# Performance work log

Measured on AMD Instinct MI355X. Metric: run time of the kernel, lower is better.

The kernel has to match this reference:

```python
import jax, jax.numpy as jnp
import numpy as np

KV_SIZE = 960
NUM_HEADS = 4
EPS = 1e-5  # InstanceNorm2d default eps
CHANNELS = [64, 128, 256, 512]
B, N = 8, 1024


def setup_inputs() -> dict:
    key = jax.random.key(0)
    ks = jax.random.split(key, 16)
    inp = {
        'emb1': jax.random.normal(ks[0], (B, N, 64), jnp.float32),
        'emb2': jax.random.normal(ks[1], (B, N, 128), jnp.float32),
        'emb3': jax.random.normal(ks[2], (B, N, 256), jnp.float32),
        'emb4': jax.random.normal(ks[3], (B, N, 512), jnp.float32),
        'emb_all': jax.random.normal(ks[4], (B, N, KV_SIZE), jnp.float32),
    }
    w = 0.02  # weight init scale
    inp['Wq1'] = jax.random.normal(ks[5], (NUM_HEADS, 64, 64), jnp.float32) * w
    inp['Wq2'] = jax.random.normal(ks[6], (NUM_HEADS, 128, 128), jnp.float32) * w
    inp['Wq3'] = jax.random.normal(ks[7], (NUM_HEADS, 256, 256), jnp.float32) * w
    inp['Wq4'] = jax.random.normal(ks[8], (NUM_HEADS, 512, 512), jnp.float32) * w
    inp['Wk'] = jax.random.normal(ks[9], (NUM_HEADS, KV_SIZE, KV_SIZE), jnp.float32) * w
    inp['Wv'] = jax.random.normal(ks[10], (NUM_HEADS, KV_SIZE, KV_SIZE), jnp.float32) * w
    inp['Wo1'] = jax.random.normal(ks[11], (64, 64), jnp.float32) * w
    inp['Wo2'] = jax.random.normal(ks[12], (128, 128), jnp.float32) * w
    inp['Wo3'] = jax.random.normal(ks[13], (256, 256), jnp.float32) * w
    inp['Wo4'] = jax.random.normal(ks[14], (512, 512), jnp.float32) * w
    return inp


def _branch(emb, Wq, K, V, Wo):
    # per-head query projection (Linear: x @ W^T), stacked over heads -> [B,H,N,C]
    Q = jnp.einsum('bnc,hdc->bhnd', emb, Wq)
    # Q^T @ K -> channel-channel scores [B,H,C,KV]
    scores = jnp.einsum('bhnc,bhnk->bhck', Q, K) / np.float32(np.sqrt(KV_SIZE))
    # InstanceNorm2d over (C,KV) per (batch, head), no affine
    mu = scores.mean(axis=(2, 3), keepdims=True)
    var = scores.var(axis=(2, 3), keepdims=True)
    scores = (scores - mu) * jax.lax.rsqrt(var + EPS)
    probs = jax.nn.softmax(scores, axis=-1)  # softmax over KV axis
    # probs @ V^T -> [B,H,C,N]; mean over heads fused into the contraction
    ctx = jnp.einsum('bhck,bhnk->bcn', probs, V) / np.float32(NUM_HEADS)
    ctx = ctx.transpose(0, 2, 1)  # [B,N,C]
    return ctx @ Wo.T  # output projection (dropout=0 -> identity)


def reference(emb1, emb2, emb3, emb4, emb_all,
              Wq1, Wq2, Wq3, Wq4, Wk, Wv, Wo1, Wo2, Wo3, Wo4):
    # shared K/V over the concatenated-channel embedding, per head: [B,H,N,KV]
    K = jnp.einsum('bnk,hok->bhno', emb_all, Wk)
    V = jnp.einsum('bnk,hok->bhno', emb_all, Wv)
    O1 = _branch(emb1, Wq1, K, V, Wo1)
    O2 = _branch(emb2, Wq2, K, V, Wo2)
    O3 = _branch(emb3, Wq3, K, V, Wo3)
    O4 = _branch(emb4, Wq4, K, V, Wo4)
    return (O1, O2, O3, O4)
```

## Files before the change

kernel.cpp:

```cpp
#include <hip/hip_runtime.h>
#include <hip/hip_bf16.h>

typedef __attribute__((ext_vector_type(8))) short short8;
typedef __attribute__((ext_vector_type(4))) float f32x4;

static __device__ __forceinline__ unsigned short f2bf(float x) {
  union { __hip_bfloat16 h; unsigned short u; } cv;
  cv.h = __float2bfloat16(x);
  return cv.u;
}

static __device__ __forceinline__ void xcd_swizzle(unsigned& bx, unsigned& by, unsigned& bz) {
  unsigned nwg = gridDim.x * gridDim.y * gridDim.z;
  unsigned lin = blockIdx.x + gridDim.x * (blockIdx.y + gridDim.y * blockIdx.z);
  unsigned chunk = nwg >> 3;
  lin = (lin & 7) * chunk + (lin >> 3);
  bx = lin % gridDim.x;
  unsigned tmp = lin / gridDim.x;
  by = tmp % gridDim.y;
  bz = tmp / gridDim.y;
}

__global__ void cast4_kernel(const float* __restrict__ s0, long n0,
                             const float* __restrict__ s1, long n1,
                             const float* __restrict__ s2, long n2,
                             const float* __restrict__ s3, long n3,
                             unsigned short* __restrict__ dst) {
  long N4 = (n0 + n1 + n2 + n3) >> 2;
  for (long i = blockIdx.x * (long)blockDim.x + threadIdx.x; i < N4;
       i += (long)gridDim.x * blockDim.x) {
    long e = i << 2;
    const float* s; long j = e;
    if (j < n0) s = s0;
    else { j -= n0; if (j < n1) s = s1;
      else { j -= n1; if (j < n2) s = s2;
        else { j -= n2; s = s3; } } }
    float4 v = *reinterpret_cast<const float4*>(s + j);
    ushort4 o;
    o.x = f2bf(v.x); o.y = f2bf(v.y); o.z = f2bf(v.z); o.w = f2bf(v.w);
    *reinterpret_cast<ushort4*>(dst + e) = o;
  }
}

__global__ __launch_bounds__(256)
void tcast_kernel(const float* __restrict__ in, unsigned short* __restrict__ out,
                  int R, int C, long sIn, long sOut) {
  __shared__ float tile[64][65];
  int z = blockIdx.z;
  const float* src = in + (long)z * sIn;
  unsigned short* dst = out + (long)z * sOut;
  int r0 = blockIdx.y * 64, c0 = blockIdx.x * 64;
  int t = threadIdx.x;
  int lr = t >> 4;
  int lc = (t & 15) * 4;
#pragma unroll
  for (int j = 0; j < 4; ++j) {
    int r = lr + j * 16;
    float4 v = *reinterpret_cast<const float4*>(src + (long)(r0 + r) * C + c0 + lc);
    tile[r][lc] = v.x; tile[r][lc + 1] = v.y; tile[r][lc + 2] = v.z; tile[r][lc + 3] = v.w;
  }
  __syncthreads();
#pragma unroll
  for (int j = 0; j < 4; ++j) {
    int oc = lr + j * 16;
    ushort4 o;
    o.x = f2bf(tile[lc][oc]);
    o.y = f2bf(tile[lc + 1][oc]);
    o.z = f2bf(tile[lc + 2][oc]);
    o.w = f2bf(tile[lc + 3][oc]);
    *reinterpret_cast<ushort4*>(dst + (long)(c0 + oc) * R + r0 + lc) = o;
  }
}

struct YDesc { int m0[8]; int mw[8]; int br[8]; };

template<int TM, int TN, int OUT, int DO_STATS, int YD>
__global__ __launch_bounds__(256)
void gemm_nt(const unsigned short* __restrict__ A,
             const unsigned short* __restrict__ B,
             void* __restrict__ Cp,
             int K, int lda, int ldb, long ldc, int Hdiv,
             long sAb, long sAh, long sBb, long sBh, long sC,
             int nInner, long iA, long iB,
             float alpha, float* __restrict__ stats,
             int Mclamp, int Nclamp, int Mwrite, int Nwrite, int Nvalid, YDesc yd) {
  constexpr int WM = TM / 32, WN = TN / 32;
  __shared__ unsigned short As[2][TM * 32];
  __shared__ unsigned short Bs[2][TN * 32];
  __shared__ float red[8];

  unsigned bxu, byu, bzu;
  xcd_swizzle(bxu, byu, bzu);
  int z = (int)bzu;
  int b = z / Hdiv, h = z % Hdiv;
  const unsigned short* Ab = A + (long)b * sAb + (long)h * sAh;
  const unsigned short* Bb = B + (long)b * sBb + (long)h * sBh;
  int y = (int)byu;
  int m0 = YD ? yd.m0[y] : y * TM;
  int rowLimit = YD ? (m0 + yd.mw[y]) : Mwrite;
  int n0 = (int)bxu * TN;
  int t = threadIdx.x;
  int lane = t & 63, wave = t >> 6;
  int wm = (wave >> 1) * (TM / 2), wn = (wave & 1) * (TN / 2);
  int l15 = lane & 15, q = lane >> 4;
  int arow = t >> 2, acol = (t & 3) * 8;

  int rA[TM / 64], rB[TN / 64];
#pragma unroll
  for (int r = 0; r < TM / 64; ++r) rA[r] = min(m0 + r * 64 + arow, Mclamp - 1);
#pragma unroll
  for (int r = 0; r < TN / 64; ++r) rB[r] = min(n0 + r * 64 + arow, Nclamp - 1);

  int kSteps = K >> 5;
  int nt = nInner * kSteps;
  const unsigned short* Asrc = Ab;
  const unsigned short* Bsrc = Bb;
  int kk = 0;

  auto stage = [&](int bufSel) {
#pragma unroll
    for (int r = 0; r < TM / 64; ++r)
      __builtin_amdgcn_global_load_lds(
          (const __attribute__((address_space(1))) void*)(Asrc + (long)rA[r] * lda + acol + kk),
          (__attribute__((address_space(3))) void*)(&As[bufSel][r * 2048 + t * 8]), 16, 0, 0);
#pragma unroll
    for (int r = 0; r < TN / 64; ++r)
      __builtin_amdgcn_global_load_lds(
          (const __attribute__((address_space(1))) void*)(Bsrc + (long)rB[r] * ldb + acol + kk),
          (__attribute__((address_space(3))) void*)(&Bs[bufSel][r * 2048 + t * 8]), 16, 0, 0);
  };
  auto advance = [&]() { kk += 32; if (kk >= K) { kk = 0; Asrc += iA; Bsrc += iB; } };

  f32x4 acc[WM][WN] = {};
  stage(0);
  advance();
  __syncthreads();
  for (int s = 0; s < nt; ++s) {
    int cur = s & 1;
    if (s + 1 < nt) { stage(cur ^ 1); advance(); }
    short8 af[WM], bfr[WN];
#pragma unroll
    for (int i = 0; i < WM; ++i)
      af[i] = *reinterpret_cast<const short8*>(&As[cur][(wm + i * 16 + l15) * 32 + q * 8]);
#pragma unroll
    for (int j = 0; j < WN; ++j)
      bfr[j] = *reinterpret_cast<const short8*>(&Bs[cur][(wn + j * 16 + l15) * 32 + q * 8]);
#pragma unroll
    for (int i = 0; i < WM; ++i)
#pragma unroll
      for (int j = 0; j < WN; ++j)
        acc[i][j] = __builtin_amdgcn_mfma_f32_16x16x32_bf16(af[i], bfr[j], acc[i][j], 0, 0, 0);
    __syncthreads();
  }

  long cbase = (long)z * sC;
  float ssum = 0.f, ssq = 0.f;
#pragma unroll
  for (int i = 0; i < WM; ++i)
#pragma unroll
    for (int j = 0; j < WN; ++j)
#pragma unroll
      for (int r = 0; r < 4; ++r) {
        float v = acc[i][j][r] * alpha;
        int rg = m0 + wm + i * 16 + q * 4 + r;
        int cg = n0 + wn + j * 16 + l15;
        if (rg < rowLimit && cg < Nwrite) {
          long idx = cbase + (long)rg * ldc + cg;
          if (OUT == 1) ((float*)Cp)[idx] = v;
          else if (OUT == 2) ((_Float16*)Cp)[idx] = (_Float16)v;
          else ((unsigned short*)Cp)[idx] = f2bf(v);
        }
        if (DO_STATS && rg < rowLimit && cg < Nvalid) { ssum += v; ssq += v * v; }
      }

  if (DO_STATS) {
#pragma unroll
    for (int o = 32; o; o >>= 1) {
      ssum += __shfl_down(ssum, o, 64);
      ssq  += __shfl_down(ssq,  o, 64);
    }
    if (lane == 0) { red[wave] = ssum; red[wave + 4] = ssq; }
    __syncthreads();
    if (t == 0) {
      long slot = YD ? ((long)z * 8 + yd.br[y] * 2) : ((long)z * 2);
      atomicAdd(stats + slot,     red[0] + red[1] + red[2] + red[3]);
      atomicAdd(stats + slot + 1, red[4] + red[5] + red[6] + red[7]);
    }
  }
}

struct BDesc { int K[8]; int aRow0[8]; int out0[8]; int mw[8]; int bc[8]; long aOff[8]; long aH[8]; };

__global__ __launch_bounds__(256)
void gemm_bd(const unsigned short* __restrict__ A0,
             const unsigned short* __restrict__ B0,
             unsigned short* __restrict__ Cp,
             int ldb, long sBz, long sC, BDesc d) {
  constexpr int TM = 128, TN = 64, WM = 4, WN = 2;
  __shared__ unsigned short As[2][TM * 32];
  __shared__ unsigned short Bs[2][TN * 32];
  unsigned bxu, byu, bzu;
  xcd_swizzle(bxu, byu, bzu);
  int z = (int)bzu;
  int b = z >> 2, h = z & 3;
  int y = (int)byu;
  int K = d.K[y];
  const unsigned short* Ab = A0 + d.aOff[y] + (long)h * d.aH[y];
  const unsigned short* Bb = B0 + (long)b * sBz + d.bc[y];
  int n0 = (int)bxu * TN;
  int t = threadIdx.x;
  int lane = t & 63, wave = t >> 6;
  int wm = (wave >> 1) * 64, wn = (wave & 1) * 32;
  int l15 = lane & 15, q = lane >> 4;
  int arow = t >> 2, acol = (t & 3) * 8;

  int rA0 = min(d.aRow0[y] + arow, K - 1);
  int rA1 = min(d.aRow0[y] + 64 + arow, K - 1);
  int rB0 = n0 + arow;

  int kk = 0;
  auto stage = [&](int bufSel) {
    __builtin_amdgcn_global_load_lds(
        (const __attribute__((address_space(1))) void*)(Ab + (long)rA0 * K + acol + kk),
        (__attribute__((address_space(3))) void*)(&As[bufSel][t * 8]), 16, 0, 0);
    __builtin_amdgcn_global_load_lds(
        (const __attribute__((address_space(1))) void*)(Ab + (long)rA1 * K + acol + kk),
        (__attribute__((address_space(3))) void*)(&As[bufSel][2048 + t * 8]), 16, 0, 0);
    __builtin_amdgcn_global_load_lds(
        (const __attribute__((address_space(1))) void*)(Bb + (long)rB0 * ldb + acol + kk),
        (__attribute__((address_space(3))) void*)(&Bs[bufSel][t * 8]), 16, 0, 0);
  };

  int nt = K >> 5;
  f32x4 acc[WM][WN] = {};
  stage(0);
  kk += 32;
  __syncthreads();
  for (int s = 0; s < nt; ++s) {
    int cur = s & 1;
    if (s + 1 < nt) { stage(cur ^ 1); kk += 32; }
    short8 af[WM], bfr[WN];
#pragma unroll
    for (int i = 0; i < WM; ++i)
      af[i] = *reinterpret_cast<const short8*>(&As[cur][(wm + i * 16 + l15) * 32 + q * 8]);
#pragma unroll
    for (int j = 0; j < WN; ++j)
      bfr[j] = *reinterpret_cast<const short8*>(&Bs[cur][(wn + j * 16 + l15) * 32 + q * 8]);
#pragma unroll
    for (int i = 0; i < WM; ++i)
#pragma unroll
      for (int j = 0; j < WN; ++j)
        acc[i][j] = __builtin_amdgcn_mfma_f32_16x16x32_bf16(af[i], bfr[j], acc[i][j], 0, 0, 0);
    __syncthreads();
  }

  long cbase = (long)z * sC;
  int mw = d.mw[y], out0 = d.out0[y];
#pragma unroll
  for (int i = 0; i < WM; ++i)
#pragma unroll
    for (int j = 0; j < WN; ++j)
#pragma unroll
      for (int r = 0; r < 4; ++r) {
        int loc = wm + i * 16 + q * 4 + r;
        int cg = n0 + wn + j * 16 + l15;
        if (loc < mw) {
          long idx = cbase + (long)(out0 + loc) * 960 + cg;
          Cp[idx] = f2bf(acc[i][j][r]);
        }
      }
}

__global__ __launch_bounds__(256)
void norm_softmax_all(_Float16* __restrict__ S, const float* __restrict__ stats) {
  long row = blockIdx.x;
  int z = (int)(row / 960), cc = (int)(row % 960);
  int br = (cc < 64) ? 0 : (cc < 192) ? 1 : (cc < 448) ? 2 : 3;
  int Cbr = (br == 0) ? 64 : (br == 1) ? 128 : (br == 2) ? 256 : 512;
  float invCnt = 1.0f / ((float)Cbr * 960.0f);
  float m1 = stats[z * 8 + br * 2 + 0] * invCnt;
  float m2 = stats[z * 8 + br * 2 + 1] * invCnt;
  float rsig = rsqrtf(m2 - m1 * m1 + 1e-5f);
  _Float16* s = S + row * 960;
  int t = threadIdx.x;
  float e[4]; float acc = 0.f;
#pragma unroll
  for (int j = 0; j < 4; ++j) {
    int i = t + j * 256;
    if (i < 960) { e[j] = __expf(((float)s[i] - m1) * rsig); acc += e[j]; }
    else e[j] = 0.f;
  }
#pragma unroll
  for (int o = 32; o; o >>= 1) acc += __shfl_down(acc, o, 64);
  __shared__ float red[4];
  if ((t & 63) == 0) red[t >> 6] = acc;
  __syncthreads();
  float inv = 1.0f / (red[0] + red[1] + red[2] + red[3]);
  unsigned short* p = (unsigned short*)s;
#pragma unroll
  for (int j = 0; j < 4; ++j) {
    int i = t + j * 256;
    if (i < 960) p[i] = f2bf(e[j] * inv);
  }
}

struct MDesc {
  long aOff[4], bOff[4], cOff[4];
  long sAz[4], sBz[4], sCz[4];
  long iA[4], iB[4];
  int  lda[4], ldb[4], ldcv[4];
  int  Kk[4], Ncl[4], nIn[4];
  int  nstart[4];
  float alpha[4];
};

template<int OUT_F32>
__global__ __launch_bounds__(256)
void gemm_multi(const unsigned short* __restrict__ A0,
                const unsigned short* __restrict__ B0,
                void* __restrict__ Cp, MDesc d) {
  __shared__ unsigned short As[2][128 * 32];
  __shared__ unsigned short Bs[2][128 * 32];
  unsigned bxu, byu, bzu;
  xcd_swizzle(bxu, byu, bzu);
  int bx = (int)bxu;
  int br = (bx >= d.nstart[3]) ? 3 : (bx >= d.nstart[2]) ? 2 : (bx >= d.nstart[1]) ? 1 : 0;
  int z = (int)bzu;
  int n0 = (bx - d.nstart[br]) * 128;
  int m0 = (int)byu * 128;
  int K = d.Kk[br], lda = d.lda[br], ldb = d.ldb[br], ldc = d.ldcv[br];
  int Ncl = d.Ncl[br], nInner = d.nIn[br];
  long iA = d.iA[br], iB = d.iB[br];
  float alpha = d.alpha[br];
  const unsigned short* Ab = A0 + d.aOff[br] + (long)z * d.sAz[br];
  const unsigned short* Bb = B0 + d.bOff[br] + (long)z * d.sBz[br];

  int t = threadIdx.x, lane = t & 63, wave = t >> 6;
  int wm = (wave >> 1) * 64, wn = (wave & 1) * 64;
  int l15 = lane & 15, q = lane >> 4;
  int arow = t >> 2, acol = (t & 3) * 8;
  int rA0 = m0 + arow, rA1 = m0 + 64 + arow;
  int rB0 = min(n0 + arow, Ncl - 1), rB1 = min(n0 + 64 + arow, Ncl - 1);

  const unsigned short* Asrc = Ab;
  const unsigned short* Bsrc = Bb;
  int kk = 0;
  auto stage = [&](int bufSel) {
    __builtin_amdgcn_global_load_lds(
        (const __attribute__((address_space(1))) void*)(Asrc + (long)rA0 * lda + acol + kk),
        (__attribute__((address_space(3))) void*)(&As[bufSel][t * 8]), 16, 0, 0);
    __builtin_amdgcn_global_load_lds(
        (const __attribute__((address_space(1))) void*)(Asrc + (long)rA1 * lda + acol + kk),
        (__attribute__((address_space(3))) void*)(&As[bufSel][2048 + t * 8]), 16, 0, 0);
    __builtin_amdgcn_global_load_lds(
        (const __attribute__((address_space(1))) void*)(Bsrc + (long)rB0 * ldb + acol + kk),
        (__attribute__((address_space(3))) void*)(&Bs[bufSel][t * 8]), 16, 0, 0);
    __builtin_amdgcn_global_load_lds(
        (const __attribute__((address_space(1))) void*)(Bsrc + (long)rB1 * ldb + acol + kk),
        (__attribute__((address_space(3))) void*)(&Bs[bufSel][2048 + t * 8]), 16, 0, 0);
  };
  auto advance = [&]() { kk += 32; if (kk >= K) { kk = 0; Asrc += iA; Bsrc += iB; } };

  int nt = nInner * (K >> 5);
  f32x4 acc[4][4] = {};
  stage(0);
  advance();
  __syncthreads();
  for (int s = 0; s < nt; ++s) {
    int cur = s & 1;
    if (s + 1 < nt) { stage(cur ^ 1); advance(); }
    short8 af[4], bfr[4];
#pragma unroll
    for (int i = 0; i < 4; ++i)
      af[i] = *reinterpret_cast<const short8*>(&As[cur][(wm + i * 16 + l15) * 32 + q * 8]);
#pragma unroll
    for (int j = 0; j < 4; ++j)
      bfr[j] = *reinterpret_cast<const short8*>(&Bs[cur][(wn + j * 16 + l15) * 32 + q * 8]);
#pragma unroll
    for (int i = 0; i < 4; ++i)
#pragma unroll
      for (int j = 0; j < 4; ++j)
        acc[i][j] = __builtin_amdgcn_mfma_f32_16x16x32_bf16(af[i], bfr[j], acc[i][j], 0, 0, 0);
    __syncthreads();
  }

  long cb = d.cOff[br] + (long)z * d.sCz[br];
#pragma unroll
  for (int i = 0; i < 4; ++i)
#pragma unroll
    for (int j = 0; j < 4; ++j)
#pragma unroll
      for (int r = 0; r < 4; ++r) {
        float v = acc[i][j][r] * alpha;
        int rg = m0 + wm + i * 16 + q * 4 + r;
        int cg = n0 + wn + j * 16 + l15;
        if (cg < Ncl) {
          long idx = cb + (long)rg * ldc + cg;
          if (OUT_F32) ((float*)Cp)[idx] = v;
          else ((unsigned short*)Cp)[idx] = f2bf(v);
        }
      }
}

extern "C" void kernel_launch(void* const* d_in, const int* in_sizes, int n_in,
                              void* d_out, int out_size, void* d_ws, size_t ws_size,
                              hipStream_t stream) {
  const float* embs[4] = {(const float*)d_in[0], (const float*)d_in[1],
                          (const float*)d_in[2], (const float*)d_in[3]};
  const float* embA = (const float*)d_in[4];
  const float* Wq1  = (const float*)d_in[5];
  const float* Wq2  = (const float*)d_in[6];
  const float* Wq3  = (const float*)d_in[7];
  const float* Wq4  = (const float*)d_in[8];
  const float* Wk   = (const float*)d_in[9];
  const float* Wv   = (const float*)d_in[10];
  float* out = (float*)d_out;

  char* base = (char*)d_ws;
  size_t off = 0;
  auto take = [&](size_t bytes) -> void* {
    void* p = base + off;
    off += (bytes + 255) & ~(size_t)255;
    return p;
  };
  unsigned short* EA    = (unsigned short*)take(15728640);
  unsigned short* embAT = (unsigned short*)take(15728640);
  unsigned short* embTc = (unsigned short*)take(15728640);
  unsigned short* WQb   = (unsigned short*)take(2785280);
  unsigned short* WKb   = (unsigned short*)take(7372800);
  unsigned short* WvT   = (unsigned short*)take(7372800);
  unsigned short* WOb   = (unsigned short*)take(696320);
  float*          ST    = (float*)take(1024);
  unsigned short* GT    = (unsigned short*)take(14745600);
  unsigned short* Tbuf  = (unsigned short*)take(58982400);
  char*           SCr   = (char*)take(58982400);
  _Float16*       SC    = (_Float16*)SCr;
  unsigned short* PR    = (unsigned short*)SCr;
  unsigned short* SPW   = GT;
  unsigned short* CT    = embAT;

  if (ws_size < off) return;

  hipMemsetAsync(ST, 0, 1024, stream);

  const long Cs[4]     = {64, 128, 256, 512};
  const long c0s[4]    = {0, 64, 192, 448};
  const long woOff[4]  = {0, 4096, 20480, 86016};
  const long outOff[4] = {0, 524288, 1572864, 3670016};
  const float kscale = 0.0322748612f;
  YDesc ydDummy = {};

  cast4_kernel<<<4096, 256, 0, stream>>>(embA, 7864320, embA, 0, embA, 0, embA, 0, EA);
  cast4_kernel<<<1024, 256, 0, stream>>>(Wq1, 16384, Wq2, 65536, Wq3, 262144, Wq4, 1048576, WQb);
  cast4_kernel<<<1024, 256, 0, stream>>>(Wk, 3686400, Wk, 0, Wk, 0, Wk, 0, WKb);
  cast4_kernel<<<512, 256, 0, stream>>>((const float*)d_in[11], 4096, (const float*)d_in[12], 16384,
                                        (const float*)d_in[13], 65536, (const float*)d_in[14], 262144, WOb);
  tcast_kernel<<<dim3(15, 16, 8), 256, 0, stream>>>(embA, embAT, 1024, 960, 983040, 983040);
  for (int i = 0; i < 4; ++i)
    tcast_kernel<<<dim3((int)Cs[i] / 64, 16, 8), 256, 0, stream>>>(
        embs[i], embTc + c0s[i] * 1024, 1024, (int)Cs[i], 1024 * Cs[i], 983040);
  tcast_kernel<<<dim3(15, 15, 4), 256, 0, stream>>>(Wv, WvT, 960, 960, 921600, 921600);

  gemm_nt<128, 128, 0, 0, 0><<<dim3(8, 8, 8), 256, 0, stream>>>(
      embAT, embTc, GT, 1024, 1024, 1024, 960, 1,
      983040L, 0L, 983040L, 0L, 921600L,
      1, 0L, 0L, 1.0f, nullptr, 960, 960, 960, 960, 0, ydDummy);

  {
    BDesc d;
    const int brOf[8]  = {0, 1, 2, 2, 3, 3, 3, 3};
    const int ar0[8]   = {0, 0, 0, 128, 0, 128, 256, 384};
    const long wqOff[4] = {0, 16384, 81920, 344064};
    for (int y = 0; y < 8; ++y) {
      int br = brOf[y];
      int Ci = (int)Cs[br];
      d.K[y] = Ci;
      d.aRow0[y] = ar0[y];
      d.out0[y] = (int)c0s[br] + ar0[y];
      d.mw[y] = (br == 0) ? 64 : 128;
      d.bc[y] = (int)c0s[br];
      d.aOff[y] = wqOff[br];
      d.aH[y] = (long)Ci * Ci;
    }
    gemm_bd<<<dim3(15, 8, 32), 256, 0, stream>>>(WQb, GT, Tbuf, 960, 921600L, 921600L, d);
  }

  {
    YDesc yd;
    const int m0s[8] = {0, 64, 192, 320, 448, 576, 704, 832};
    const int mws[8] = {64, 128, 128, 128, 128, 128, 128, 128};
    const int brs[8] = {0, 1, 2, 2, 3, 3, 3, 3};
    for (int y = 0; y < 8; ++y) { yd.m0[y] = m0s[y]; yd.mw[y] = mws[y]; yd.br[y] = brs[y]; }
    gemm_nt<128, 128, 2, 1, 1><<<dim3(8, 8, 32), 256, 0, stream>>>(
        Tbuf, WKb, SC, 960, 960, 960, 960, 4,
        3686400L, 921600L, 0L, 921600L, 921600L,
        1, 0L, 0L, kscale, ST, 960, 960, 960, 960, 960, yd);
  }

  norm_softmax_all<<<dim3(32 * 960), 256, 0, stream>>>(SC, ST);

  gemm_nt<128, 128, 0, 0, 0><<<dim3(8, 8, 8), 256, 0, stream>>>(
      PR, WvT, SPW, 960, 960, 960, 960, 1,
      3686400L, 0L, 0L, 0L, 921600L,
      4, 921600L, 921600L, 0.25f, nullptr, 960, 960, 960, 960, 0, ydDummy);

  gemm_nt<128, 128, 0, 0, 0><<<dim3(8, 8, 8), 256, 0, stream>>>(
      EA, SPW, CT, 960, 960, 960, 960, 1,
      983040L, 0L, 921600L, 0L, 983040L,
      1, 0L, 0L, 1.0f, nullptr, 1024, 960, 1024, 960, 0, ydDummy);

  {
    MDesc d;
    for (int i = 0; i < 4; ++i) {
      long C = Cs[i];
      d.aOff[i] = c0s[i];       d.sAz[i] = 983040L;          d.iA[i] = 0;
      d.bOff[i] = woOff[i];     d.sBz[i] = 0;                d.iB[i] = 0;
      d.cOff[i] = outOff[i];    d.sCz[i] = 1024L * C;
      d.lda[i] = 960; d.ldb[i] = (int)C; d.ldcv[i] = (int)C;
      d.Kk[i] = (int)C; d.Ncl[i] = (int)C; d.nIn[i] = 1;
      d.alpha[i] = 1.0f;
    }
    d.nstart[0] = 0; d.nstart[1] = 1; d.nstart[2] = 2; d.nstart[3] = 4;
    gemm_multi<1><<<dim3(8, 8, 8), 256, 0, stream>>>(CT, WOb, out, d);
  }
  (void)in_sizes; (void)n_in; (void)out_size;
}
```

Baseline: 513.8 us.

## Deepen GEMM LDS pipeline to four buffers with two-stage prefetch and vmcnt waits

```diff
diff --git a/kernel.cpp b/kernel.cpp
--- a/kernel.cpp
+++ b/kernel.cpp
@@ -8,6 +8,14 @@
   union { __hip_bfloat16 h; unsigned short u; } cv;
   cv.h = __float2bfloat16(x);
   return cv.u;
+}
+
+template<int N> static __device__ __forceinline__ void waitcnt_vm() {
+  if constexpr (N == 0) asm volatile("s_waitcnt vmcnt(0)" ::: "memory");
+  else if constexpr (N == 3) asm volatile("s_waitcnt vmcnt(3)" ::: "memory");
+  else if constexpr (N == 4) asm volatile("s_waitcnt vmcnt(4)" ::: "memory");
+  else if constexpr (N == 6) asm volatile("s_waitcnt vmcnt(6)" ::: "memory");
+  else if constexpr (N == 8) asm volatile("s_waitcnt vmcnt(8)" ::: "memory");
 }
 
 static __device__ __forceinline__ void xcd_swizzle(unsigned& bx, unsigned& by, unsigned& bz) {
@@ -85,8 +93,9 @@
              float alpha, float* __restrict__ stats,
              int Mclamp, int Nclamp, int Mwrite, int Nwrite, int Nvalid, YDesc yd) {
   constexpr int WM = TM / 32, WN = TN / 32;
-  __shared__ unsigned short As[2][TM * 32];
-  __shared__ unsigned short Bs[2][TN * 32];
+  constexpr int L = TM / 64 + TN / 64;
+  __shared__ unsigned short As[4][TM * 32];
+  __shared__ unsigned short Bs[4][TN * 32];
   __shared__ float red[8];
 
   unsigned bxu, byu, bzu;
@@ -128,29 +137,34 @@
       __builtin_amdgcn_global_load_lds(
           (const __attribute__((address_space(1))) void*)(Bsrc + (long)rB[r] * ldb + acol + kk),
           (__attribute__((address_space(3))) void*)(&Bs[bufSel][r * 2048 + t * 8]), 16, 0, 0);
+    kk += 32; if (kk >= K) { kk = 0; Asrc += iA; Bsrc += iB; }
   };
-  auto advance = [&]() { kk += 32; if (kk >= K) { kk = 0; Asrc += iA; Bsrc += iB; } };
 
   f32x4 acc[WM][WN] = {};
   stage(0);
-  advance();
-  __syncthreads();
+  if (nt > 1) stage(1);
   for (int s = 0; s < nt; ++s) {
-    int cur = s & 1;
-    if (s + 1 < nt) { stage(cur ^ 1); advance(); }
+    if (s + 2 < nt) stage((s + 2) & 3);
+    int rem = nt - 1 - s;
+    if (rem >= 2) waitcnt_vm<2 * L>();
+    else if (rem == 1) waitcnt_vm<L>();
+    else waitcnt_vm<0>();
+    __builtin_amdgcn_s_barrier();
+    __builtin_amdgcn_sched_barrier(0);
+    const unsigned short* Ac = As[s & 3];
+    const unsigned short* Bc = Bs[s & 3];
     short8 af[WM], bfr[WN];
 #pragma unroll
     for (int i = 0; i < WM; ++i)
-      af[i] = *reinterpret_cast<const short8*>(&As[cur][(wm + i * 16 + l15) * 32 + q * 8]);
+      af[i] = *reinterpret_cast<const short8*>(Ac + (wm + i * 16 + l15) * 32 + q * 8);
 #pragma unroll
     for (int j = 0; j < WN; ++j)
-      bfr[j] = *reinterpret_cast<const short8*>(&Bs[cur][(wn + j * 16 + l15) * 32 + q * 8]);
+      bfr[j] = *reinterpret_cast<const short8*>(Bc + (wn + j * 16 + l15) * 32 + q * 8);
 #pragma unroll
     for (int i = 0; i < WM; ++i)
 #pragma unroll
       for (int j = 0; j < WN; ++j)
         acc[i][j] = __builtin_amdgcn_mfma_f32_16x16x32_bf16(af[i], bfr[j], acc[i][j], 0, 0, 0);
-    __syncthreads();
   }
 
   long cbase = (long)z * sC;
@@ -197,8 +211,8 @@
              unsigned short* __restrict__ Cp,
              int ldb, long sBz, long sC, BDesc d) {
   constexpr int TM = 128, TN = 64, WM = 4, WN = 2;
-  __shared__ unsigned short As[2][TM * 32];
-  __shared__ unsigned short Bs[2][TN * 32];
+  __shared__ unsigned short As[4][TM * 32];
+  __shared__ unsigned short Bs[4][TN * 32];
   unsigned bxu, byu, bzu;
   xcd_swizzle(bxu, byu, bzu);
   int z = (int)bzu;
@@ -229,29 +243,35 @@
     __builtin_amdgcn_global_load_lds(
         (const __attribute__((address_space(1))) void*)(Bb + (long)rB0 * ldb + acol + kk),
         (__attribute__((address_space(3))) void*)(&Bs[bufSel][t * 8]), 16, 0, 0);
+    kk += 32;
   };
 
   int nt = K >> 5;
   f32x4 acc[WM][WN] = {};
   stage(0);
-  kk += 32;
-  __syncthreads();
+  if (nt > 1) stage(1);
   for (int s = 0; s < nt; ++s) {
-    int cur = s & 1;
-    if (s + 1 < nt) { stage(cur ^ 1); kk += 32; }
+    if (s + 2 < nt) stage((s + 2) & 3);
+    int rem = nt - 1 - s;
+    if (rem >= 2) waitcnt_vm<6>();
+    else if (rem == 1) waitcnt_vm<3>();
+    else waitcnt_vm<0>();
+    __builtin_amdgcn_s_barrier();
+    __builtin_amdgcn_sched_barrier(0);
+    const unsigned short* Ac = As[s & 3];
+    const unsigned short* Bc = Bs[s & 3];
     short8 af[WM], bfr[WN];
 #pragma unroll
     for (int i = 0; i < WM; ++i)
-      af[i] = *reinterpret_cast<const short8*>(&As[cur][(wm + i * 16 + l15) * 32 + q * 8]);
+      af[i] = *reinterpret_cast<const short8*>(Ac + (wm + i * 16 + l15) * 32 + q * 8);
 #pragma unroll
     for (int j = 0; j < WN; ++j)
-      bfr[j] = *reinterpret_cast<const short8*>(&Bs[cur][(wn + j * 16 + l15) * 32 + q * 8]);
+      bfr[j] = *reinterpret_cast<const short8*>(Bc + (wn + j * 16 + l15) * 32 + q * 8);
 #pragma unroll
     for (int i = 0; i < WM; ++i)
 #pragma unroll
       for (int j = 0; j < WN; ++j)
         acc[i][j] = __builtin_amdgcn_mfma_f32_16x16x32_bf16(af[i], bfr[j], acc[i][j], 0, 0, 0);
-    __syncthreads();
   }
 
   long cbase = (long)z * sC;
@@ -319,8 +339,8 @@
 void gemm_multi(const unsigned short* __restrict__ A0,
                 const unsigned short* __restrict__ B0,
                 void* __restrict__ Cp, MDesc d) {
-  __shared__ unsigned short As[2][128 * 32];
-  __shared__ unsigned short Bs[2][128 * 32];
+  __shared__ unsigned short As[4][128 * 32];
+  __shared__ unsigned short Bs[4][128 * 32];
   unsigned bxu, byu, bzu;
   xcd_swizzle(bxu, byu, bzu);
   int bx = (int)bxu;
@@ -358,30 +378,35 @@
     __builtin_amdgcn_global_load_lds(
         (const __attribute__((address_space(1))) void*)(Bsrc + (long)rB1 * ldb + acol + kk),
         (__attribute__((address_space(3))) void*)(&Bs[bufSel][2048 + t * 8]), 16, 0, 0);
+    kk += 32; if (kk >= K) { kk = 0; Asrc += iA; Bsrc += iB; }
   };
-  auto advance = [&]() { kk += 32; if (kk >= K) { kk = 0; Asrc += iA; Bsrc += iB; } };
 
   int nt = nInner * (K >> 5);
   f32x4 acc[4][4] = {};
   stage(0);
-  advance();
-  __syncthreads();
+  if (nt > 1) stage(1);
   for (int s = 0; s < nt; ++s) {
-    int cur = s & 1;
-    if (s + 1 < nt) { stage(cur ^ 1); advance(); }
+    if (s + 2 < nt) stage((s + 2) & 3);
+    int rem = nt - 1 - s;
+    if (rem >= 2) waitcnt_vm<8>();
+    else if (rem == 1) waitcnt_vm<4>();
+    else waitcnt_vm<0>();
+    __builtin_amdgcn_s_barrier();
+    __builtin_amdgcn_sched_barrier(0);
+    const unsigned short* Ac = As[s & 3];
+    const unsigned short* Bc = Bs[s & 3];
     short8 af[4], bfr[4];
 #pragma unroll
     for (int i = 0; i < 4; ++i)
-      af[i] = *reinterpret_cast<const short8*>(&As[cur][(wm + i * 16 + l15) * 32 + q * 8]);
+      af[i] = *reinterpret_cast<const short8*>(Ac + (wm + i * 16 + l15) * 32 + q * 8);
 #pragma unroll
     for (int j = 0; j < 4; ++j)
-      bfr[j] = *reinterpret_cast<const short8*>(&Bs[cur][(wn + j * 16 + l15) * 32 + q * 8]);
+      bfr[j] = *reinterpret_cast<const short8*>(Bc + (wn + j * 16 + l15) * 32 + q * 8);
 #pragma unroll
     for (int i = 0; i < 4; ++i)
 #pragma unroll
       for (int j = 0; j < 4; ++j)
         acc[i][j] = __builtin_amdgcn_mfma_f32_16x16x32_bf16(af[i], bfr[j], acc[i][j], 0, 0, 0);
-    __syncthreads();
   }
 
   long cb = d.cOff[br] + (long)z * d.sCz[br];
```

New measurement: 512.3 us. About the same (-0.3%).
